# Kernel tuning notes

Measured on AMD Instinct MI355X. Metric: run time of the kernel, lower is better.

The kernel has to match this reference:

```python
import jax, jax.numpy as jnp
import numpy as np

N, C, H, W = 4, 15, 320, 320
FEATS_OUT, KSIZE, PAD, CONV_PAD, K_RBF = 32, 11, 11, 5, 31
VMAX = 1.0


def _fft2c(x):
    # fastMRI-style centered orthonormal 2D FFT on complex array [..., H, W]
    x = jnp.fft.ifftshift(x, axes=(-2, -1))
    x = jnp.fft.fft2(x, axes=(-2, -1), norm='ortho')
    return jnp.fft.fftshift(x, axes=(-2, -1))


def _ifft2c(x):
    x = jnp.fft.ifftshift(x, axes=(-2, -1))
    x = jnp.fft.ifft2(x, axes=(-2, -1), norm='ortho')
    return jnp.fft.fftshift(x, axes=(-2, -1))


def _to_c(x):
    return jax.lax.complex(x[..., 0], x[..., 1])


def _to_r(z):
    return jnp.stack([jnp.real(z), jnp.imag(z)], axis=-1)


def setup_inputs() -> dict:
    key = jax.random.key(0)
    ks = jax.random.split(key, 8)
    u_t = jax.random.normal(ks[0], (N, H, W, 2), dtype=jnp.float32)
    f = jax.random.normal(ks[1], (N, C, H, W, 2), dtype=jnp.float32)
    coil_sens = jax.random.normal(ks[2], (N, C, H, W, 2), dtype=jnp.float32)
    sampling_mask = (jax.random.uniform(ks[3], (N, H, W)) < 0.35).astype(jnp.float32)
    conv_kernel = jax.random.normal(ks[4], (FEATS_OUT, 1, KSIZE, KSIZE, 2), dtype=jnp.float32)
    conv_kernel = conv_kernel / np.sqrt(KSIZE * KSIZE * 2 * 1)
    conv_kernel = conv_kernel - jnp.mean(conv_kernel, axis=(1, 2, 3, 4), keepdims=True)
    x0 = jnp.linspace(-VMAX, VMAX, K_RBF, dtype=jnp.float32)
    w = jnp.broadcast_to((0.04 * x0).reshape(1, 1, 1, 1, K_RBF), (1, FEATS_OUT, 1, 1, K_RBF)).astype(jnp.float32)
    mu = x0
    sigma = jnp.array([2.0 * VMAX / (K_RBF - 1)], dtype=jnp.float32)
    lamb = jnp.array([1.0], dtype=jnp.float32)
    return {'u_t': u_t, 'f': f, 'coil_sens': coil_sens, 'sampling_mask': sampling_mask,
            'conv_kernel': conv_kernel, 'w': w, 'mu': mu, 'sigma': sigma, 'lamb': lamb}


def reference(u_t, f, coil_sens, sampling_mask, conv_kernel, w, mu, sigma, lamb):
    dn = ('NCHW', 'OIHW', 'NCHW')
    feats_out = conv_kernel.shape[0]
    k = conv_kernel.shape[2]

    # --- regularizer: reflect-pad, complex conv pair, RBF activation, transposed conv pair ---
    pad_cfg = ((0, 0), (0, 0), (PAD, PAD), (PAD, PAD))
    ur = jnp.pad(u_t[:, None, :, :, 0], pad_cfg, mode='reflect')  # [N,1,Hp,Wp]
    ui = jnp.pad(u_t[:, None, :, :, 1], pad_cfg, mode='reflect')

    def conv(x, Wk):
        return jax.lax.conv_general_dilated(x, Wk, (1, 1), [(CONV_PAD, CONV_PAD)] * 2,
                                            dimension_numbers=dn)

    u_k = conv(ur, conv_kernel[..., 0]) + conv(ui, conv_kernel[..., 1])  # [N,Co,Hp,Wp]

    # RBF activation: sum_i w_i * exp(-(x - mu_i)^2 / (2 sigma^2)), scanned over centers
    wk = jnp.transpose(w[0, :, 0, 0, :])  # [K, Co]
    inv2s2 = 1.0 / (2.0 * sigma[0] ** 2)

    def body(acc, wm):
        wi, mi = wm
        acc = acc + wi[None, :, None, None] * jnp.exp(-jnp.square(u_k - mi) * inv2s2)
        return acc, None

    f_u_k, _ = jax.lax.scan(body, jnp.zeros_like(u_k), (wk, mu))

    # conv_transpose2d(padding=CONV_PAD) == conv with flipped kernel, swapped channels, padding k-1-CONV_PAD
    tpad = k - 1 - CONV_PAD

    def convT(x, Wk):
        Wt = jnp.transpose(Wk[:, :, ::-1, ::-1], (1, 0, 2, 3))  # [I,O,k,k] -> OIHW w/ O=1
        return jax.lax.conv_general_dilated(x, Wt, (1, 1), [(tpad, tpad)] * 2,
                                            dimension_numbers=dn)

    Ru_r = convT(f_u_k, conv_kernel[..., 0])[:, 0]  # [N,Hp,Wp]
    Ru_i = convT(f_u_k, conv_kernel[..., 1])[:, 0]
    Ru = jnp.stack([Ru_r, Ru_i], axis=-1)[:, PAD:-PAD, PAD:-PAD, :] / feats_out  # [N,H,W,2]

    # --- data consistency: A^T (A u - f) (cartesian, os=False) ---
    u_c = _to_c(u_t)              # [N,H,W]
    c_c = _to_c(coil_sens)        # [N,C,H,W]
    f_c = _to_c(f)                # [N,C,H,W]
    m = sampling_mask[:, None]    # [N,1,H,W]
    Au = m * _fft2c(u_c[:, None] * c_c)
    At = jnp.sum(_ifft2c(m * (Au - f_c)) * jnp.conj(c_c), axis=1)  # [N,H,W]
    Du = _to_r(At) * lamb[0]

    return u_t - Ru - Du
```

## Files before the change

### kernel.cpp

```cpp
#include <hip/hip_runtime.h>
#include <hip/hip_bf16.h>
#include <math.h>

#define NN 4
#define CC 15
#define HH 320
#define WW 320
#define HW (HH*WW)
#define FF 32
#define KS 11
#define PADN 11
#define CPAD 5
#define HP 342
#define NK 31
#define NCB (NN*CC)
#define TABN 256

typedef short bf16x8 __attribute__((ext_vector_type(8)));
typedef float f32x4 __attribute__((ext_vector_type(4)));
typedef unsigned short u16x4 __attribute__((ext_vector_type(4)));

#define MFMA16 __builtin_amdgcn_mfma_f32_16x16x32_bf16

__device__ __forceinline__ unsigned int pack_bf(float r, float i) {
  __hip_bfloat16 hr = __float2bfloat16(r), hi = __float2bfloat16(i);
  unsigned short ur = *(unsigned short*)&hr, ui = *(unsigned short*)&hi;
  return (unsigned int)ur | ((unsigned int)ui << 16);
}
__device__ __forceinline__ unsigned short f2b(float x) {
  __hip_bfloat16 h = __float2bfloat16(x);
  return *(unsigned short*)&h;
}
__device__ __forceinline__ float b2f(unsigned short u) {
  __hip_bfloat16 h = *(__hip_bfloat16*)&u;
  return __bfloat162float(h);
}
__device__ __forceinline__ unsigned int rot16(unsigned int x) {
  return (x >> 16) | (x << 16);
}
__device__ __forceinline__ bf16x8 xf4(uint4 p, unsigned int x) {
  union { unsigned int u[4]; bf16x8 v; } t;
  t.u[0] = p.x ^ x; t.u[1] = p.y ^ x; t.u[2] = p.z ^ x; t.u[3] = p.w ^ x;
  return t.v;
}
__device__ __forceinline__ bf16x8 xr4(uint4 p, unsigned int x) {
  union { unsigned int u[4]; bf16x8 v; } t;
  t.u[0] = rot16(p.x) ^ x; t.u[1] = rot16(p.y) ^ x;
  t.u[2] = rot16(p.z) ^ x; t.u[3] = rot16(p.w) ^ x;
  return t.v;
}
__device__ __forceinline__ size_t pk_idx(int row, int col) {
  return (size_t)((row >> 4) * 20 + (col >> 4)) * 256 + (row & 15) * 16 + (col & 15);
}

__global__ void k_dft(unsigned int* __restrict__ Fpk) {
  int idx = blockIdx.x * blockDim.x + threadIdx.x;
  if (idx >= HW) return;
  int k = idx / WW, n = idx % WW;
  int prod = (k - 160) * (n - 160);
  int r = prod % 320; if (r < 0) r += 320;
  float ang = -6.283185307179586f * (float)r / 320.0f;
  const float s = 0.05590169943749474f;
  Fpk[pk_idx(k, n)] = pack_bf(cosf(ang) * s, sinf(ang) * s);
}

__global__ void k_prep(const float* __restrict__ ck, unsigned int* __restrict__ Wpk) {
  int idx = blockIdx.x * blockDim.x + threadIdx.x;
  if (idx >= 32 * 176) return;
  int o = idx / 176, kw = idx % 176;
  int ky = kw / 16, kx = kw % 16;
  unsigned int v = 0;
  if (kx <= 10) {
    const float* p = &ck[(o * 121 + ky * 11 + kx) * 2];
    v = pack_bf(p[0], p[1]);
  }
  Wpk[idx] = v;
}

__global__ void k_prep2(const float* __restrict__ ck, unsigned short* __restrict__ Wt) {
  int idx = blockIdx.x * blockDim.x + threadIdx.x;
  if (idx >= 2 * 11 * 16 * 32) return;
  int o = idx & 31;
  int ky = (idx >> 5) & 15;
  int rest = idx >> 9;
  int kx = rest % 11, ch = rest / 11;
  unsigned short v = 0;
  if (ky <= 10) v = f2b(ck[(o * 121 + ky * 11 + kx) * 2 + ch]);
  Wt[idx] = v;
}

__global__ void k_rbftab(const float* __restrict__ w, const float* __restrict__ mu,
                         const float* __restrict__ sigma, unsigned short* __restrict__ Tab) {
  int o = blockIdx.x;
  int e = threadIdx.x;
  if (e >= TABN + 1) return;
  float v = -2.0f + (float)e * (4.0f / (float)TABN);
  float sg = sigma[0];
  float nInv = -1.0f / (2.0f * sg * sg);
  float acc = 0.f;
  for (int i = 0; i < NK; i++) {
    float d = v - mu[i];
    acc += w[o * NK + i] * __expf(d * d * nInv);
  }
  Tab[o * 260 + e] = f2b(acc);
}

__global__ __launch_bounds__(256) void k_conv_rbf_mfma(
    const float* __restrict__ u_t, const unsigned int* __restrict__ Wpk,
    const unsigned short* __restrict__ Tab, unsigned short* __restrict__ fukT) {
  __shared__ unsigned int lW[32 * 180];
  __shared__ unsigned int tIn[26 * 32];
  __shared__ unsigned short tab[32 * 260];
  int n = blockIdx.z;
  int y0 = blockIdx.y * 16, x0 = blockIdx.x * 16;
  int tid = threadIdx.x;
  for (int i = tid; i < 32 * 176; i += 256)
    lW[(i / 176) * 180 + (i % 176)] = Wpk[i];
  {
    const unsigned int* Ts = (const unsigned int*)Tab;
    unsigned int* Td = (unsigned int*)tab;
    for (int i = tid; i < 32 * 130; i += 256) Td[i] = Ts[i];
  }
  for (int i = tid; i < 26 * 32; i += 256) {
    int rr = i >> 5, cc = i & 31;
    unsigned int v = 0;
    if (cc < 26) {
      int py = y0 + rr - 5, px = x0 + cc - 5;
      if (py >= 0 && py < HP && px >= 0 && px < HP) {
        int uy = py - PADN; uy = uy < 0 ? -uy : (uy >= HH ? 2 * (HH - 1) - uy : uy);
        int ux = px - PADN; ux = ux < 0 ? -ux : (ux >= WW ? 2 * (WW - 1) - ux : ux);
        const float* up = &u_t[((n * HH + uy) * WW + ux) * 2];
        v = pack_bf(up[0], up[1]);
      }
    }
    tIn[i] = v;
  }
  __syncthreads();
  int lane = tid & 63, wave = tid >> 6;
  int m16 = lane & 15, kq = lane >> 4;
  const short* lWs = (const short*)lW;
  f32x4 acc[4][2] = {};
  for (int ky = 0; ky < 11; ky++) {
    bf16x8 af0 = *(const bf16x8*)&lWs[m16 * 360 + ky * 32 + kq * 8];
    bf16x8 af1 = *(const bf16x8*)&lWs[(m16 + 16) * 360 + ky * 32 + kq * 8];
    #pragma unroll
    for (int nt = 0; nt < 4; nt++) {
      int rr = wave * 4 + nt + ky;
      int c0 = rr * 32 + m16 + kq * 4;
      union { unsigned int u[4]; bf16x8 v; } bu;
      bu.u[0] = tIn[c0]; bu.u[1] = tIn[c0 + 1];
      bu.u[2] = tIn[c0 + 2]; bu.u[3] = tIn[c0 + 3];
      acc[nt][0] = MFMA16(af0, bu.v, acc[nt][0], 0, 0, 0);
      acc[nt][1] = MFMA16(af1, bu.v, acc[nt][1], 0, 0, 0);
    }
  }
  const float tscale = (float)TABN / 4.0f;
  #pragma unroll
  for (int nt = 0; nt < 4; nt++) {
    int Y = y0 + wave * 4 + nt;
    int X = x0 + m16;
    if (Y >= HP || X >= HP) continue;
    #pragma unroll
    for (int mt = 0; mt < 2; mt++) {
      u16x4 pk;
      #pragma unroll
      for (int r = 0; r < 4; r++) {
        float v = acc[nt][mt][r];
        int o = mt * 16 + kq * 4 + r;
        float t = (v + 2.0f) * tscale;
        t = fminf(fmaxf(t, 0.0f), 255.999f);
        int i0 = (int)t;
        float fr = t - (float)i0;
        float a = b2f(tab[o * 260 + i0]);
        float bv = b2f(tab[o * 260 + i0 + 1]);
        pk[r] = f2b(a + (bv - a) * fr);
      }
      *(u16x4*)&fukT[(((size_t)n * HP + Y) * HP + X) * 32 + mt * 16 + kq * 4] = pk;
    }
  }
}

__global__ __launch_bounds__(256) void k_convT_mfma(
    const unsigned short* __restrict__ fukT, const unsigned short* __restrict__ Wt,
    float* __restrict__ Ru) {
  __shared__ unsigned short rowBuf[42 * 32];
  __shared__ float accS[16 * 67];
  int n = blockIdx.z;
  int y0 = blockIdx.y * 16, x0 = blockIdx.x * 32;
  int tid = threadIdx.x;
  int lane = tid & 63, wave = tid >> 6;
  int ch = wave >> 1, xh = wave & 1;
  int m16 = lane & 15, kq = lane >> 4;
  bf16x8 afr[11];
  #pragma unroll
  for (int kx = 0; kx < 11; kx++)
    afr[kx] = *(const bf16x8*)&Wt[((ch * 11 + kx) * 16 + m16) * 32 + kq * 8];
  for (int i = tid; i < 16 * 67; i += 256) accS[i] = 0.f;
  int xl = xh * 16 + m16;
  for (int t = 0; t < 26; t++) {
    int r = y0 + 6 + t;
    __syncthreads();
    {
      const unsigned int* src = (const unsigned int*)&fukT[(((size_t)n * HP + r) * HP + x0 + 6) * 32];
      unsigned int* dst = (unsigned int*)rowBuf;
      for (int i = tid; i < 42 * 16; i += 256) dst[i] = src[i];
    }
    __syncthreads();
    f32x4 dacc = {};
    #pragma unroll
    for (int kx = 0; kx < 11; kx++) {
      bf16x8 bfrag = *(const bf16x8*)&rowBuf[(xl + 10 - kx) * 32 + kq * 8];
      dacc = MFMA16(afr[kx], bfrag, dacc, 0, 0, 0);
    }
    #pragma unroll
    for (int rg = 0; rg < 4; rg++) {
      int ky = kq * 4 + rg;
      int y = t + ky - 10;
      if (ky <= 10 && y >= 0 && y < 16)
        accS[y * 67 + xl * 2 + ch] += dacc[rg];
    }
  }
  __syncthreads();
  int chO = tid & 1, xO = (tid >> 1) & 31, yb = tid >> 6;
  #pragma unroll
  for (int q = 0; q < 4; q++) {
    int y = yb + q * 4;
    Ru[(((size_t)n * HH + y0 + y) * WW + x0 + xO) * 2 + chO] = accS[y * 67 + xO * 2 + chO];
  }
}

__global__ __launch_bounds__(256) void k_umulT(const float* __restrict__ u_t,
                                               const float* __restrict__ cs,
                                               unsigned int* __restrict__ X0T) {
  __shared__ unsigned int t[32 * 33];
  int bc = blockIdx.x;
  int b = blockIdx.y;
  int n = b / CC;
  int ty = (bc / 10) * 32, tx = (bc % 10) * 32;
  int r = threadIdx.x >> 5, c = threadIdx.x & 31;
  #pragma unroll
  for (int q = 0; q < 4; q++) {
    int y = ty + r + q * 8, x = tx + c;
    const float* up = &u_t[((size_t)n * HW + (size_t)y * WW + x) * 2];
    const float* cp = &cs[((size_t)b * HW + (size_t)y * WW + x) * 2];
    float ur = up[0], ui = up[1], crr = cp[0], cii = cp[1];
    t[(r + q * 8) * 33 + c] = pack_bf(ur * crr - ui * cii, ur * cii + ui * crr);
  }
  __syncthreads();
  #pragma unroll
  for (int q = 0; q < 4; q++) {
    int xx = r + q * 8;
    int x = tx + xx, y = ty + c;
    X0T[(size_t)b * HW + pk_idx(x, y)] = t[c * 33 + xx];
  }
}

template <int MODE>
__global__ __launch_bounds__(256, 4) void k_dcpair(
    const unsigned int* __restrict__ Fpk,
    const unsigned int* __restrict__ Bp,
    const float* __restrict__ mask, const float* __restrict__ fdat,
    unsigned int* __restrict__ Out) {
  __shared__ unsigned int sMem[5440];
  int bid = blockIdx.x;
  int wg = (bid & 7) * 150 + (bid >> 3);
  int b = wg / 20, strip = wg % 20;
  int i0 = strip * 16;
  int tid = threadIdx.x;
  int lane = tid & 63, wc = tid >> 6;
  int m16 = lane & 15, kq = lane >> 4;
  int loff = m16 * 16 + kq * 4;
  const unsigned int XA1 = (MODE == 1) ? 0x80000000u : 0u;
  const unsigned int XA2 = (MODE == 1) ? 0u : 0x00008000u;

  const unsigned int* Ap = Fpk + (size_t)strip * 5120 + loff;
  const unsigned int* Bb = Bp + (size_t)b * HW + (size_t)(wc * 5) * 5120 + loff;

  f32x4 aR[5] = {}, aI[5] = {};
  uint4 a0 = *(const uint4*)&Ap[0];
  uint4 a1v = *(const uint4*)&Ap[256];
  uint4 b0[5], b1[5];
  #pragma unroll
  for (int ct = 0; ct < 5; ct++) {
    b0[ct] = *(const uint4*)&Bb[ct * 5120];
    b1[ct] = *(const uint4*)&Bb[ct * 5120 + 256];
  }
  #pragma unroll
  for (int kc2 = 0; kc2 < 10; kc2++) {
    {
      const int kc = kc2 * 2;
      bf16x8 x1 = xf4(a0, XA1), x2 = xr4(a0, XA2);
      bf16x8 bc[5];
      #pragma unroll
      for (int ct = 0; ct < 5; ct++) bc[ct] = *(const bf16x8*)&b0[ct];
      if (kc + 2 < 20) {
        a0 = *(const uint4*)&Ap[(kc + 2) * 256];
        #pragma unroll
        for (int ct = 0; ct < 5; ct++)
          b0[ct] = *(const uint4*)&Bb[ct * 5120 + (kc + 2) * 256];
      }
      #pragma unroll
      for (int ct = 0; ct < 5; ct++) {
        aR[ct] = MFMA16(x1, bc[ct], aR[ct], 0, 0, 0);
        aI[ct] = MFMA16(x2, bc[ct], aI[ct], 0, 0, 0);
      }
    }
    {
      const int kc = kc2 * 2 + 1;
      bf16x8 x1 = xf4(a1v, XA1), x2 = xr4(a1v, XA2);
      bf16x8 bc[5];
      #pragma unroll
      for (int ct = 0; ct < 5; ct++) bc[ct] = *(const bf16x8*)&b1[ct];
      if (kc + 2 < 20) {
        a1v = *(const uint4*)&Ap[(kc + 2) * 256];
        #pragma unroll
        for (int ct = 0; ct < 5; ct++)
          b1[ct] = *(const uint4*)&Bb[ct * 5120 + (kc + 2) * 256];
      }
      #pragma unroll
      for (int ct = 0; ct < 5; ct++) {
        aR[ct] = MFMA16(x1, bc[ct], aR[ct], 0, 0, 0);
        aI[ct] = MFMA16(x2, bc[ct], aI[ct], 0, 0, 0);
      }
    }
  }
  #pragma unroll
  for (int ct = 0; ct < 5; ct++)
    #pragma unroll
    for (int r = 0; r < 4; r++) {
      int trow = kq * 4 + r;
      int tcol = wc * 80 + ct * 16 + m16;
      unsigned int v = pack_bf(aR[ct][r], aI[ct][r]);
      if (MODE == 2) v ^= 0x80000000u;
      sMem[trow * 340 + tcol] = v;
    }
  __syncthreads();

  f32x4 cR[5] = {}, cI[5] = {};
  const unsigned int* Tr = &sMem[m16 * 340];
  const unsigned int* Fb = Fpk + (size_t)(wc * 5) * 5120 + loff;
  uint4 tp = *(const uint4*)&Tr[kq * 4];
  uint4 fp[5];
  #pragma unroll
  for (int ct = 0; ct < 5; ct++) fp[ct] = *(const uint4*)&Fb[ct * 5120];
  #pragma unroll
  for (int kc = 0; kc < 20; kc++) {
    bf16x8 x1 = xf4(tp, 0x80000000u), x2 = xr4(tp, 0u);
    bf16x8 bc[5];
    #pragma unroll
    for (int ct = 0; ct < 5; ct++) bc[ct] = *(const bf16x8*)&fp[ct];
    if (kc < 19) {
      tp = *(const uint4*)&Tr[(kc + 1) * 16 + kq * 4];
      #pragma unroll
      for (int ct = 0; ct < 5; ct++)
        fp[ct] = *(const uint4*)&Fb[ct * 5120 + (kc + 1) * 256];
    }
    #pragma unroll
    for (int ct = 0; ct < 5; ct++) {
      cR[ct] = MFMA16(x1, bc[ct], cR[ct], 0, 0, 0);
      cI[ct] = MFMA16(x2, bc[ct], cI[ct], 0, 0, 0);
    }
  }

  if constexpr (MODE == 1) {
    __syncthreads();
    int n = b / CC;
    #pragma unroll
    for (int ct = 0; ct < 5; ct++)
      #pragma unroll
      for (int r = 0; r < 4; r++) {
        int row = i0 + kq * 4 + r;
        int col = wc * 80 + ct * 16 + m16;
        float m = mask[n * HW + row * WW + col];
        size_t fi = ((size_t)b * HW + (size_t)row * WW + col) * 2;
        float vr = m * (cR[ct][r] - fdat[fi]);
        float vi = m * (cI[ct][r] - fdat[fi + 1]);
        sMem[col * 17 + kq * 4 + r] = pack_bf(vr, vi);
      }
    __syncthreads();
    for (int i2 = tid; i2 < 320 * 16; i2 += 256) {
      int x = i2 >> 4, yy = i2 & 15;
      Out[(size_t)b * HW + pk_idx(x, i0 + yy)] = sMem[x * 17 + yy];
    }
  } else {
    #pragma unroll
    for (int ct = 0; ct < 5; ct++)
      #pragma unroll
      for (int r = 0; r < 4; r++) {
        int row = i0 + kq * 4 + r;
        int col = wc * 80 + ct * 16 + m16;
        Out[(size_t)b * HW + (size_t)row * WW + col] =
            pack_bf(cR[ct][r], cI[ct][r]) ^ 0x80000000u;
      }
  }
}

__global__ void k_coilsum(const unsigned int* __restrict__ Z, const float* __restrict__ cs,
                          float* __restrict__ At) {
  int idx = blockIdx.x * blockDim.x + threadIdx.x;
  if (idx >= NN * HW) return;
  int n = idx / HW, hw = idx % HW;
  float ar = 0.f, ai = 0.f;
  for (int c = 0; c < CC; c++) {
    size_t zi = (size_t)(n * CC + c) * HW + hw;
    unsigned int p = Z[zi];
    float zr = b2f((unsigned short)(p & 0xffff));
    float zim = b2f((unsigned short)(p >> 16));
    float crr = cs[zi * 2], cii = cs[zi * 2 + 1];
    ar += zr * crr + zim * cii;
    ai += zim * crr - zr * cii;
  }
  At[idx * 2] = ar;
  At[idx * 2 + 1] = ai;
}

__global__ void k_final(const float* __restrict__ u_t, const float* __restrict__ Ru,
                        const float* __restrict__ At, const float* __restrict__ lamb,
                        float* __restrict__ out) {
  int idx = blockIdx.x * blockDim.x + threadIdx.x;
  if (idx >= NN * HW * 2) return;
  out[idx] = u_t[idx] - Ru[idx] * (1.0f / (float)FF) - lamb[0] * At[idx];
}

extern "C" void kernel_launch(void* const* d_in, const int* in_sizes, int n_in,
                              void* d_out, int out_size, void* d_ws, size_t ws_size,
                              hipStream_t stream) {
  const float* u_t   = (const float*)d_in[0];
  const float* fdat  = (const float*)d_in[1];
  const float* cs    = (const float*)d_in[2];
  const float* mask  = (const float*)d_in[3];
  const float* ck    = (const float*)d_in[4];
  const float* w     = (const float*)d_in[5];
  const float* mu    = (const float*)d_in[6];
  const float* sigma = (const float*)d_in[7];
  const float* lamb  = (const float*)d_in[8];
  float* out = (float*)d_out;

  unsigned int* wsw = (unsigned int*)d_ws;
  unsigned int* Fpk = wsw;
  unsigned int* Wpk = wsw + 102400;
  unsigned short* Wt = (unsigned short*)(wsw + 108160);
  unsigned short* Tab = (unsigned short*)(wsw + 113792);
  float* At = (float*)(wsw + 117952);
  float* Ru = (float*)(wsw + 937152);
  unsigned int* big = wsw + 1756352;
  unsigned short* fukT = (unsigned short*)big;
  unsigned int* X0T = big;
  unsigned int* P2T = big + 6144000;
  unsigned int* Q = big;

  k_dft<<<(HW + 255) / 256, 256, 0, stream>>>(Fpk);
  k_prep<<<(32 * 176 + 255) / 256, 256, 0, stream>>>(ck, Wpk);
  k_prep2<<<(2 * 11 * 16 * 32 + 255) / 256, 256, 0, stream>>>(ck, Wt);
  k_rbftab<<<32, 320, 0, stream>>>(w, mu, sigma, Tab);
  k_conv_rbf_mfma<<<dim3(22, 22, NN), 256, 0, stream>>>(u_t, Wpk, Tab, fukT);
  k_convT_mfma<<<dim3(10, 20, NN), 256, 0, stream>>>(fukT, Wt, Ru);
  k_umulT<<<dim3(100, 60), 256, 0, stream>>>(u_t, cs, X0T);
  k_dcpair<1><<<1200, 256, 0, stream>>>(Fpk, X0T, mask, fdat, P2T);
  k_dcpair<2><<<1200, 256, 0, stream>>>(Fpk, P2T, nullptr, nullptr, Q);
  k_coilsum<<<(NN * HW + 255) / 256, 256, 0, stream>>>(Q, cs, At);
  k_final<<<(NN * HW * 2 + 255) / 256, 256, 0, stream>>>(u_t, Ru, At, lamb, out);
}
```

Before: 424.1 us.

## Double dcpair row-strip height to 32 and stage DFT rows in LDS

The DFT-pair kernel now has each workgroup handle a 32-row strip instead of 16, so each B-operand fragment fetched from global memory feeds twice as many MFMAs. The block's DFT-matrix rows are first copied into shared memory and the A fragments are read from there. The grid is halved to 600 blocks, LDS use grows and the occupancy hint drops to 2 blocks per CU, and accumulator register pressure doubles. This risks lower occupancy and less latency hiding in exchange for fewer redundant global loads.

```diff
diff --git a/kernel.cpp b/kernel.cpp
--- a/kernel.cpp
+++ b/kernel.cpp
@@ -256,16 +256,16 @@
 }
 
 template <int MODE>
-__global__ __launch_bounds__(256, 4) void k_dcpair(
+__global__ __launch_bounds__(256, 2) void k_dcpair(
     const unsigned int* __restrict__ Fpk,
     const unsigned int* __restrict__ Bp,
     const float* __restrict__ mask, const float* __restrict__ fdat,
     unsigned int* __restrict__ Out) {
-  __shared__ unsigned int sMem[5440];
+  __shared__ unsigned int sMem[10560];
   int bid = blockIdx.x;
-  int wg = (bid & 7) * 150 + (bid >> 3);
-  int b = wg / 20, strip = wg % 20;
-  int i0 = strip * 16;
+  int wg = (bid & 7) * 75 + (bid >> 3);
+  int b = wg / 10, strip = wg % 10;
+  int i0 = strip * 32;
   int tid = threadIdx.x;
   int lane = tid & 63, wc = tid >> 6;
   int m16 = lane & 15, kq = lane >> 4;
@@ -273,92 +273,152 @@
   const unsigned int XA1 = (MODE == 1) ? 0x80000000u : 0u;
   const unsigned int XA2 = (MODE == 1) ? 0u : 0x00008000u;
 
-  const unsigned int* Ap = Fpk + (size_t)strip * 5120 + loff;
   const unsigned int* Bb = Bp + (size_t)b * HW + (size_t)(wc * 5) * 5120 + loff;
 
-  f32x4 aR[5] = {}, aI[5] = {};
-  uint4 a0 = *(const uint4*)&Ap[0];
-  uint4 a1v = *(const uint4*)&Ap[256];
   uint4 b0[5], b1[5];
   #pragma unroll
   for (int ct = 0; ct < 5; ct++) {
     b0[ct] = *(const uint4*)&Bb[ct * 5120];
     b1[ct] = *(const uint4*)&Bb[ct * 5120 + 256];
   }
+  {
+    const uint4* src = (const uint4*)(Fpk + (size_t)strip * 10240);
+    #pragma unroll
+    for (int q = 0; q < 10; q++)
+      *(uint4*)&sMem[q * 1024 + tid * 4] = src[q * 256 + tid];
+  }
+  __syncthreads();
+
+  f32x4 aR0[5] = {}, aI0[5] = {}, aR1[5] = {}, aI1[5] = {};
+  uint4 ac0 = *(const uint4*)&sMem[loff];
+  uint4 ac1 = *(const uint4*)&sMem[5120 + loff];
   #pragma unroll
   for (int kc2 = 0; kc2 < 10; kc2++) {
     {
       const int kc = kc2 * 2;
-      bf16x8 x1 = xf4(a0, XA1), x2 = xr4(a0, XA2);
+      uint4 an0 = *(const uint4*)&sMem[(kc + 1) * 256 + loff];
+      uint4 an1 = *(const uint4*)&sMem[5120 + (kc + 1) * 256 + loff];
+      bf16x8 x10 = xf4(ac0, XA1), x20 = xr4(ac0, XA2);
+      bf16x8 x11 = xf4(ac1, XA1), x21 = xr4(ac1, XA2);
       bf16x8 bc[5];
       #pragma unroll
       for (int ct = 0; ct < 5; ct++) bc[ct] = *(const bf16x8*)&b0[ct];
       if (kc + 2 < 20) {
-        a0 = *(const uint4*)&Ap[(kc + 2) * 256];
         #pragma unroll
         for (int ct = 0; ct < 5; ct++)
           b0[ct] = *(const uint4*)&Bb[ct * 5120 + (kc + 2) * 256];
       }
       #pragma unroll
       for (int ct = 0; ct < 5; ct++) {
-        aR[ct] = MFMA16(x1, bc[ct], aR[ct], 0, 0, 0);
-        aI[ct] = MFMA16(x2, bc[ct], aI[ct], 0, 0, 0);
-      }
+        aR0[ct] = MFMA16(x10, bc[ct], aR0[ct], 0, 0, 0);
+        aI0[ct] = MFMA16(x20, bc[ct], aI0[ct], 0, 0, 0);
+        aR1[ct] = MFMA16(x11, bc[ct], aR1[ct], 0, 0, 0);
+        aI1[ct] = MFMA16(x21, bc[ct], aI1[ct], 0, 0, 0);
+      }
+      ac0 = an0; ac1 = an1;
     }
     {
       const int kc = kc2 * 2 + 1;
-      bf16x8 x1 = xf4(a1v, XA1), x2 = xr4(a1v, XA2);
+      uint4 an0, an1;
+      if (kc + 1 < 20) {
+        an0 = *(const uint4*)&sMem[(kc + 1) * 256 + loff];
+        an1 = *(const uint4*)&sMem[5120 + (kc + 1) * 256 + loff];
+      }
+      bf16x8 x10 = xf4(ac0, XA1), x20 = xr4(ac0, XA2);
+      bf16x8 x11 = xf4(ac1, XA1), x21 = xr4(ac1, XA2);
       bf16x8 bc[5];
       #pragma unroll
       for (int ct = 0; ct < 5; ct++) bc[ct] = *(const bf16x8*)&b1[ct];
       if (kc + 2 < 20) {
-        a1v = *(const uint4*)&Ap[(kc + 2) * 256];
         #pragma unroll
         for (int ct = 0; ct < 5; ct++)
           b1[ct] = *(const uint4*)&Bb[ct * 5120 + (kc + 2) * 256];
       }
       #pragma unroll
       for (int ct = 0; ct < 5; ct++) {
-        aR[ct] = MFMA16(x1, bc[ct], aR[ct], 0, 0, 0);
-        aI[ct] = MFMA16(x2, bc[ct], aI[ct], 0, 0, 0);
-      }
-    }
-  }
+        aR0[ct] = MFMA16(x10, bc[ct], aR0[ct], 0, 0, 0);
+        aI0[ct] = MFMA16(x20, bc[ct], aI0[ct], 0, 0, 0);
+        aR1[ct] = MFMA16(x11, bc[ct], aR1[ct], 0, 0, 0);
+        aI1[ct] = MFMA16(x21, bc[ct], aI1[ct], 0, 0, 0);
+      }
+      if (kc + 1 < 20) { ac0 = an0; ac1 = an1; }
+    }
+  }
+
+  __syncthreads();
   #pragma unroll
   for (int ct = 0; ct < 5; ct++)
     #pragma unroll
     for (int r = 0; r < 4; r++) {
-      int trow = kq * 4 + r;
-      int tcol = wc * 80 + ct * 16 + m16;
-      unsigned int v = pack_bf(aR[ct][r], aI[ct][r]);
-      if (MODE == 2) v ^= 0x80000000u;
-      sMem[trow * 340 + tcol] = v;
+      unsigned int v0 = pack_bf(aR0[ct][r], aI0[ct][r]);
+      unsigned int v1 = pack_bf(aR1[ct][r], aI1[ct][r]);
+      if (MODE == 2) { v0 ^= 0x80000000u; v1 ^= 0x80000000u; }
+      int w = (kq * 4 + r) * 16 + m16;
+      sMem[(wc * 5 + ct) * 256 + w] = v0;
+      sMem[(20 + wc * 5 + ct) * 256 + w] = v1;
     }
   __syncthreads();
 
-  f32x4 cR[5] = {}, cI[5] = {};
-  const unsigned int* Tr = &sMem[m16 * 340];
+  f32x4 cR0[5] = {}, cI0[5] = {}, cR1[5] = {}, cI1[5] = {};
   const unsigned int* Fb = Fpk + (size_t)(wc * 5) * 5120 + loff;
-  uint4 tp = *(const uint4*)&Tr[kq * 4];
-  uint4 fp[5];
-  #pragma unroll
-  for (int ct = 0; ct < 5; ct++) fp[ct] = *(const uint4*)&Fb[ct * 5120];
-  #pragma unroll
-  for (int kc = 0; kc < 20; kc++) {
-    bf16x8 x1 = xf4(tp, 0x80000000u), x2 = xr4(tp, 0u);
-    bf16x8 bc[5];
-    #pragma unroll
-    for (int ct = 0; ct < 5; ct++) bc[ct] = *(const bf16x8*)&fp[ct];
-    if (kc < 19) {
-      tp = *(const uint4*)&Tr[(kc + 1) * 16 + kq * 4];
-      #pragma unroll
-      for (int ct = 0; ct < 5; ct++)
-        fp[ct] = *(const uint4*)&Fb[ct * 5120 + (kc + 1) * 256];
-    }
-    #pragma unroll
-    for (int ct = 0; ct < 5; ct++) {
-      cR[ct] = MFMA16(x1, bc[ct], cR[ct], 0, 0, 0);
-      cI[ct] = MFMA16(x2, bc[ct], cI[ct], 0, 0, 0);
+  uint4 f0[5], f1[5];
+  #pragma unroll
+  for (int ct = 0; ct < 5; ct++) {
+    f0[ct] = *(const uint4*)&Fb[ct * 5120];
+    f1[ct] = *(const uint4*)&Fb[ct * 5120 + 256];
+  }
+  uint4 tc0 = *(const uint4*)&sMem[loff];
+  uint4 tc1 = *(const uint4*)&sMem[5120 + loff];
+  #pragma unroll
+  for (int kc2 = 0; kc2 < 10; kc2++) {
+    {
+      const int kc = kc2 * 2;
+      uint4 tn0 = *(const uint4*)&sMem[(kc + 1) * 256 + loff];
+      uint4 tn1 = *(const uint4*)&sMem[5120 + (kc + 1) * 256 + loff];
+      bf16x8 x10 = xf4(tc0, 0x80000000u), x20 = xr4(tc0, 0u);
+      bf16x8 x11 = xf4(tc1, 0x80000000u), x21 = xr4(tc1, 0u);
+      bf16x8 bc[5];
+      #pragma unroll
+      for (int ct = 0; ct < 5; ct++) bc[ct] = *(const bf16x8*)&f0[ct];
+      if (kc + 2 < 20) {
+        #pragma unroll
+        for (int ct = 0; ct < 5; ct++)
+          f0[ct] = *(const uint4*)&Fb[ct * 5120 + (kc + 2) * 256];
+      }
+      #pragma unroll
+      for (int ct = 0; ct < 5; ct++) {
+        cR0[ct] = MFMA16(x10, bc[ct], cR0[ct], 0, 0, 0);
+        cI0[ct] = MFMA16(x20, bc[ct], cI0[ct], 0, 0, 0);
+        cR1[ct] = MFMA16(x11, bc[ct], cR1[ct], 0, 0, 0);
+        cI1[ct] = MFMA16(x21, bc[ct], cI1[ct], 0, 0, 0);
+      }
+      tc0 = tn0; tc1 = tn1;
+    }
+    {
+      const int kc = kc2 * 2 + 1;
+      uint4 tn0, tn1;
+      if (kc + 1 < 20) {
+        tn0 = *(const uint4*)&sMem[(kc + 1) * 256 + loff];
+        tn1 = *(const uint4*)&sMem[5120 + (kc + 1) * 256 + loff];
+      }
+      bf16x8 x10 = xf4(tc0, 0x80000000u), x20 = xr4(tc0, 0u);
+      bf16x8 x11 = xf4(tc1, 0x80000000u), x21 = xr4(tc1, 0u);
+      bf16x8 bc[5];
+      #pragma unroll
+      for (int ct = 0; ct < 5; ct++) bc[ct] = *(const bf16x8*)&f1[ct];
+      if (kc + 2 < 20) {
+        #pragma unroll
+        for (int ct = 0; ct < 5; ct++)
+          f1[ct] = *(const uint4*)&Fb[ct * 5120 + (kc + 2) * 256];
+      }
+      #pragma unroll
+      for (int ct = 0; ct < 5; ct++) {
+        cR0[ct] = MFMA16(x10, bc[ct], cR0[ct], 0, 0, 0);
+        cI0[ct] = MFMA16(x20, bc[ct], cI0[ct], 0, 0, 0);
+        cR1[ct] = MFMA16(x11, bc[ct], cR1[ct], 0, 0, 0);
+        cI1[ct] = MFMA16(x21, bc[ct], cI1[ct], 0, 0, 0);
+      }
+      if (kc + 1 < 20) { tc0 = tn0; tc1 = tn1; }
     }
   }
 
@@ -369,28 +429,41 @@
     for (int ct = 0; ct < 5; ct++)
       #pragma unroll
       for (int r = 0; r < 4; r++) {
-        int row = i0 + kq * 4 + r;
         int col = wc * 80 + ct * 16 + m16;
-        float m = mask[n * HW + row * WW + col];
-        size_t fi = ((size_t)b * HW + (size_t)row * WW + col) * 2;
-        float vr = m * (cR[ct][r] - fdat[fi]);
-        float vi = m * (cI[ct][r] - fdat[fi + 1]);
-        sMem[col * 17 + kq * 4 + r] = pack_bf(vr, vi);
+        {
+          int lrow = kq * 4 + r, row = i0 + lrow;
+          float m = mask[n * HW + row * WW + col];
+          size_t fi = ((size_t)b * HW + (size_t)row * WW + col) * 2;
+          float vr = m * (cR0[ct][r] - fdat[fi]);
+          float vi = m * (cI0[ct][r] - fdat[fi + 1]);
+          sMem[col * 33 + lrow] = pack_bf(vr, vi);
+        }
+        {
+          int lrow = 16 + kq * 4 + r, row = i0 + lrow;
+          float m = mask[n * HW + row * WW + col];
+          size_t fi = ((size_t)b * HW + (size_t)row * WW + col) * 2;
+          float vr = m * (cR1[ct][r] - fdat[fi]);
+          float vi = m * (cI1[ct][r] - fdat[fi + 1]);
+          sMem[col * 33 + lrow] = pack_bf(vr, vi);
+        }
       }
     __syncthreads();
-    for (int i2 = tid; i2 < 320 * 16; i2 += 256) {
-      int x = i2 >> 4, yy = i2 & 15;
-      Out[(size_t)b * HW + pk_idx(x, i0 + yy)] = sMem[x * 17 + yy];
+    for (int i2 = tid; i2 < 320 * 32; i2 += 256) {
+      int x = i2 >> 5, yy = i2 & 31;
+      Out[(size_t)b * HW + pk_idx(x, i0 + yy)] = sMem[x * 33 + yy];
     }
   } else {
     #pragma unroll
     for (int ct = 0; ct < 5; ct++)
       #pragma unroll
       for (int r = 0; r < 4; r++) {
-        int row = i0 + kq * 4 + r;
         int col = wc * 80 + ct * 16 + m16;
-        Out[(size_t)b * HW + (size_t)row * WW + col] =
-            pack_bf(cR[ct][r], cI[ct][r]) ^ 0x80000000u;
+        int row0 = i0 + kq * 4 + r;
+        int row1 = i0 + 16 + kq * 4 + r;
+        Out[(size_t)b * HW + (size_t)row0 * WW + col] =
+            pack_bf(cR0[ct][r], cI0[ct][r]) ^ 0x80000000u;
+        Out[(size_t)b * HW + (size_t)row1 * WW + col] =
+            pack_bf(cR1[ct][r], cI1[ct][r]) ^ 0x80000000u;
       }
   }
 }
@@ -456,8 +529,8 @@
   k_conv_rbf_mfma<<<dim3(22, 22, NN), 256, 0, stream>>>(u_t, Wpk, Tab, fukT);
   k_convT_mfma<<<dim3(10, 20, NN), 256, 0, stream>>>(fukT, Wt, Ru);
   k_umulT<<<dim3(100, 60), 256, 0, stream>>>(u_t, cs, X0T);
-  k_dcpair<1><<<1200, 256, 0, stream>>>(Fpk, X0T, mask, fdat, P2T);
-  k_dcpair<2><<<1200, 256, 0, stream>>>(Fpk, P2T, nullptr, nullptr, Q);
+  k_dcpair<1><<<600, 256, 0, stream>>>(Fpk, X0T, mask, fdat, P2T);
+  k_dcpair<2><<<600, 256, 0, stream>>>(Fpk, P2T, nullptr, nullptr, Q);
   k_coilsum<<<(NN * HW + 255) / 256, 256, 0, stream>>>(Q, cs, At);
   k_final<<<(NN * HW * 2 + 255) / 256, 256, 0, stream>>>(u_t, Ru, At, lamb, out);
 }
```

New measurement: 388.7 us. 8.3% less time.
